# Kernel tuning notes

Hardware: AMD Instinct MI355X
Metric: run time of the kernel (lower is better)

## Reference

```python
import math
import jax, jax.numpy as jnp
import numpy as np

H = 8
DIM = 256
HD = DIM // H
SCALE = math.sqrt(HD)
EPS = 1e-16


def _segment_softmax(scores, dst, num_nodes):
    # scores: [E, H], dst: [E] -> softmax over edges sharing the same dst
    m = jax.ops.segment_max(scores, dst, num_segments=num_nodes)  # [N, H]
    m = jnp.where(jnp.isfinite(m), m, 0.0)  # empty segments -> -inf -> 0
    e = jnp.exp(scores - m[dst])
    s = jax.ops.segment_sum(e, dst, num_segments=num_nodes)  # [N, H]
    return e / (s[dst] + EPS)


def _graph_attention(x, edges, wq, bq, wk, bk, wv, bv, wo, bo):
    # x: [N, DIM]; edges: [2, E] (src, dst). Dropout is identity (eval mode).
    N = x.shape[0]
    Q = (x @ wq + bq).reshape(N, H, HD)
    K = (x @ wk + bk).reshape(N, H, HD)
    V = (x @ wv + bv).reshape(N, H, HD)
    src, dst = edges[0], edges[1]
    scores = jnp.einsum('ehd,ehd->eh', Q[dst], K[src]) / SCALE  # [E, H]
    attn = _segment_softmax(scores, dst, N)  # [E, H]
    msgs = V[src] * attn[:, :, None]  # [E, H, HD]
    out = jax.ops.segment_sum(msgs, dst, num_segments=N).reshape(N, DIM)
    return out @ wo + bo


def _linear_params(key, fan_in, fan_out):
    k1, k2 = jax.random.split(key)
    bound = 1.0 / math.sqrt(fan_in)
    w = jax.random.uniform(k1, (fan_in, fan_out), minval=-bound, maxval=bound, dtype=jnp.float32)
    b = jax.random.uniform(k2, (fan_out,), minval=-bound, maxval=bound, dtype=jnp.float32)
    return w, b


def setup_inputs() -> dict:
    key = jax.random.key(0)
    ks = jax.random.split(key, 12)
    n_slot, n_dom = 20000, 1000
    e_slot, e_dom = 320000, 16000
    inp = {
        'slot_x': jax.random.normal(ks[0], (n_slot, DIM), dtype=jnp.float32),
        'domain_x': jax.random.normal(ks[1], (n_dom, DIM), dtype=jnp.float32),
        'slot_edges': jax.random.randint(ks[2], (2, e_slot), 0, n_slot, dtype=jnp.int32),
        'domain_edges': jax.random.randint(ks[3], (2, e_dom), 0, n_dom, dtype=jnp.int32),
    }
    names = ['wq', 'wk', 'wv', 'wo']
    for i, nm in enumerate(names):
        w, b = _linear_params(ks[4 + i], DIM, DIM)
        inp[f'slot_{nm}'] = w
        inp[f'slot_{nm}_b'] = b
    for i, nm in enumerate(names):
        w, b = _linear_params(ks[8 + i], DIM, DIM)
        inp[f'dom_{nm}'] = w
        inp[f'dom_{nm}_b'] = b
    return inp


def reference(slot_x, domain_x, slot_edges, domain_edges,
              slot_wq, slot_wq_b, slot_wk, slot_wk_b, slot_wv, slot_wv_b, slot_wo, slot_wo_b,
              dom_wq, dom_wq_b, dom_wk, dom_wk_b, dom_wv, dom_wv_b, dom_wo, dom_wo_b):
    # slot branch: self-attention on slot graph + identity residual
    slot_out = _graph_attention(slot_x, slot_edges,
                                slot_wq, slot_wq_b, slot_wk, slot_wk_b,
                                slot_wv, slot_wv_b, slot_wo, slot_wo_b) + slot_x
    # domain branch
    dom_out = _graph_attention(domain_x, domain_edges,
                               dom_wq, dom_wq_b, dom_wk, dom_wk_b,
                               dom_wv, dom_wv_b, dom_wo, dom_wo_b) + domain_x
    return slot_out, dom_out
```

## Files before the change

### kernel.cpp

```cpp
#include <hip/hip_runtime.h>
#include <hip/hip_bf16.h>

#define DIM 256
#define INV_SCALE 0.17677669529663687f
#define SM_EPS 1e-16f
#define BM 128
#define BN 64
#define BK 32

typedef unsigned short ushortT;
typedef unsigned int uintT;
typedef __attribute__((ext_vector_type(8))) __bf16 bf16x8;
typedef __attribute__((ext_vector_type(4))) float f32x4;

__device__ __forceinline__ float bf2f(ushortT u) {
    return __uint_as_float(((uintT)u) << 16);
}
__device__ __forceinline__ ushortT f2bf(float f) {
    uintT u = __float_as_uint(f);
    u += 0x7FFFu + ((u >> 16) & 1u);
    return (ushortT)(u >> 16);
}

struct WPack { const void* w[8]; const void* b[8]; };

__device__ __forceinline__ bool sniff_m16(const ushortT* __restrict__ x) {
    int lane = threadIdx.x & 63;
    ushortT u = x[lane * 2];
    int e = (u >> 7) & 0xFF;
    bool sane = ((u & 0x7FFFu) == 0) || (e >= 0x66 && e <= 0x90);
    unsigned long long m = __ballot(sane);
    return __popcll(m) >= 32;
}

__global__ __launch_bounds__(256) void megaA(
        const void* __restrict__ xs, const void* __restrict__ xd,
        const ushortT* __restrict__ sniff_src,
        ushortT* __restrict__ xb_s, ushortT* __restrict__ xb_d,
        WPack pk, ushortT* __restrict__ wT, float* __restrict__ biasF,
        int* __restrict__ cnt_s, int* __restrict__ cnt_d,
        uintT* __restrict__ st_s, uintT* __restrict__ st_d,
        int* __restrict__ done, int* __restrict__ flagWs,
        int n4s, int n4d, int Ns_, int Nd_, int nbN_, int nbD_,
        int nA0, int nA1, int nA2)
{
    const bool m16 = sniff_m16(sniff_src);
    const int bid = blockIdx.x;
    const int t = threadIdx.x;

    if (bid < nA0 + nA1) {
        const bool d = bid >= nA0;
        const int li = d ? bid - nA0 : bid;
        const int n4 = d ? n4d : n4s;
        const int i = li * 256 + t;
        if (i >= n4) return;
        const void* x = d ? xd : xs;
        ushortT* xb = d ? xb_d : xb_s;
        if (m16) {
            ((ushort4*)xb)[i] = ((const ushort4*)x)[i];
        } else {
            float4 v = ((const float4*)x)[i];
            ushort4 o2;
            o2.x = f2bf(v.x); o2.y = f2bf(v.y); o2.z = f2bf(v.z); o2.w = f2bf(v.w);
            ((ushort4*)xb)[i] = o2;
        }
    } else if (bid < nA0 + nA1 + nA2) {
        const int r = bid - (nA0 + nA1);
        const int which = r / 257;
        const int j = r % 257;
        if (j == 256) {
            const void* b = pk.b[which];
            float v = m16 ? bf2f(((const ushortT*)b)[t]) : ((const float*)b)[t];
            biasF[which * 256 + t] = v;
        } else {
            const void* w = pk.w[which];
            float v = m16 ? bf2f(((const ushortT*)w)[t * 256 + j])
                          : ((const float*)w)[t * 256 + j];
            wT[(size_t)which * 65536 + j * 256 + t] = f2bf(v);
        }
    } else {
        const int li = bid - (nA0 + nA1 + nA2);
        const int idx = li * 256 + t;
        if (idx < Ns_) { cnt_s[idx] = 0; return; }
        int k = idx - Ns_;
        if (k < Nd_) { cnt_d[k] = 0; return; }
        k -= Nd_;
        if (k < nbN_) { st_s[k] = 0; return; }
        k -= nbN_;
        if (k < nbD_) { st_d[k] = 0; return; }
        k -= nbD_;
        if (k == 0) *done = 0;
        else if (k == 1) *flagWs = m16 ? 1 : 0;
    }
}

__device__ __forceinline__ void gemm_core(const ushortT* __restrict__ A,
                                          const ushortT* __restrict__ BT,
                                          int row0, int col0, int M,
                                          f32x4 (&acc)[2][4]) {
    __shared__ ushortT As[BM * BK];
    __shared__ ushortT Bs[BN * BK];
    const int tid  = threadIdx.x;
    const int wid  = tid >> 6;
    const int lane = tid & 63;
    const int r_i = tid >> 2;
    const int kq8 = (tid & 3) << 3;
    const int m   = lane & 15;
    const int q   = lane >> 4;

    const size_t rA0 = (size_t)min(row0 + r_i, M - 1) * DIM;
    const size_t rA1 = (size_t)min(row0 + 64 + r_i, M - 1) * DIM;
    const size_t rB  = (size_t)(col0 + r_i) * DIM;

    for (int k0 = 0; k0 < DIM; k0 += BK) {
        uint4 a0v = *(const uint4*)(A + rA0 + k0 + kq8);
        uint4 a1v = *(const uint4*)(A + rA1 + k0 + kq8);
        uint4 bv  = *(const uint4*)(BT + rB + k0 + kq8);
        __syncthreads();
        *(uint4*)&As[r_i * BK + kq8]        = a0v;
        *(uint4*)&As[(64 + r_i) * BK + kq8] = a1v;
        *(uint4*)&Bs[r_i * BK + kq8]        = bv;
        __syncthreads();

        bf16x8 af0 = *(const bf16x8*)&As[(wid * 32 + m) * BK + q * 8];
        bf16x8 af1 = *(const bf16x8*)&As[(wid * 32 + 16 + m) * BK + q * 8];
        #pragma unroll
        for (int j = 0; j < 4; ++j) {
            bf16x8 bf = *(const bf16x8*)&Bs[(j * 16 + m) * BK + q * 8];
            acc[0][j] = __builtin_amdgcn_mfma_f32_16x16x32_bf16(af0, bf, acc[0][j], 0, 0, 0);
            acc[1][j] = __builtin_amdgcn_mfma_f32_16x16x32_bf16(af1, bf, acc[1][j], 0, 0, 0);
        }
    }
}

__global__ __launch_bounds__(256) void megaB(
        const ushortT* __restrict__ xb_s, const ushortT* __restrict__ xb_d,
        const ushortT* __restrict__ wT, const float* __restrict__ biasF,
        ushortT* __restrict__ qkv_s, ushortT* __restrict__ qkv_d,
        size_t zss, size_t zsd, int Ms, int Md, int nbs_, int nbq_,
        const int* __restrict__ dst_s, const int* __restrict__ dst_d,
        int* __restrict__ cnt_s, int* __restrict__ cnt_d, int Es_, int Ed_)
{
    const int bid = blockIdx.x;
    const int nq = nbq_ * 12;
    if (bid >= nq) {
        const int idx = (bid - nq) * 256 + threadIdx.x;
        if (idx < Es_) atomicAdd(&cnt_s[dst_s[idx]], 1);
        else { int e = idx - Es_; if (e < Ed_) atomicAdd(&cnt_d[dst_d[e]], 1); }
        return;
    }
    const int z  = bid / (nbq_ * 4);
    const int r  = bid % (nbq_ * 4);
    const int by = r / nbq_;
    const int bx0 = r % nbq_;
    const bool dom = bx0 >= nbs_;
    const int bx = dom ? bx0 - nbs_ : bx0;
    const ushortT* A = dom ? xb_d : xb_s;
    const int M = dom ? Md : Ms;
    const int widx = z + (dom ? 4 : 0);
    const ushortT* BT = wT + (size_t)widx * 65536;
    const float* bias = biasF + widx * 256;
    ushortT* C = (dom ? qkv_d : qkv_s) + (size_t)z * (dom ? zsd : zss);

    const int row0 = bx * BM;
    const int col0 = by * BN;
    const int wid = threadIdx.x >> 6, lane = threadIdx.x & 63;
    const int m = lane & 15, q = lane >> 4;

    f32x4 acc[2][4];
    #pragma unroll
    for (int i = 0; i < 2; ++i)
        #pragma unroll
        for (int j = 0; j < 4; ++j) acc[i][j] = (f32x4){0.f, 0.f, 0.f, 0.f};

    gemm_core(A, BT, row0, col0, M, acc);

    #pragma unroll
    for (int i = 0; i < 2; ++i)
        #pragma unroll
        for (int j = 0; j < 4; ++j) {
            const int col = col0 + j * 16 + m;
            const float bval = bias[col];
            #pragma unroll
            for (int rr = 0; rr < 4; ++rr) {
                const int row = row0 + wid * 32 + i * 16 + q * 4 + rr;
                if (row < M)
                    C[(size_t)row * DIM + col] = f2bf(acc[i][j][rr] + bval);
            }
        }
}

__device__ __forceinline__ uintT spack(uintT st, uintT v) { return (st << 30) | v; }

__global__ __launch_bounds__(256) void scan_nodes(
        const int* __restrict__ cnt_s, const int* __restrict__ cnt_d,
        uintT* __restrict__ st_s, uintT* __restrict__ st_d,
        int* __restrict__ rp_s, int* __restrict__ rp_d,
        int* __restrict__ cur_s, int* __restrict__ cur_d,
        int Ns_, int Nd_, int nbN_)
{
    __shared__ int sh[256];
    __shared__ int exclS;
    const int b = blockIdx.x;
    const int t = threadIdx.x;
    const bool dom = b >= nbN_;
    const int lb = dom ? b - nbN_ : b;
    const int N = dom ? Nd_ : Ns_;
    const int* cnt = dom ? cnt_d : cnt_s;
    uintT* st = dom ? st_d : st_s;
    int* rp = dom ? rp_d : rp_s;
    int* cur = dom ? cur_d : cur_s;

    const int i = lb * 256 + t;
    const int v = (i < N) ? cnt[i] : 0;
    sh[t] = v;
    __syncthreads();
    for (int off = 1; off < 256; off <<= 1) {
        int u = (t >= off) ? sh[t - off] : 0;
        __syncthreads();
        sh[t] += u;
        __syncthreads();
    }

    if (t == 0) {
        const uintT agg = (uintT)sh[255];
        uintT excl = 0;
        if (lb == 0) {
            __hip_atomic_store(&st[0], spack(2u, agg), __ATOMIC_RELEASE,
                               __HIP_MEMORY_SCOPE_AGENT);
        } else {
            __hip_atomic_store(&st[lb], spack(1u, agg), __ATOMIC_RELEASE,
                               __HIP_MEMORY_SCOPE_AGENT);
            int j = lb - 1;
            while (j >= 0) {
                uintT s = __hip_atomic_load(&st[j], __ATOMIC_ACQUIRE,
                                            __HIP_MEMORY_SCOPE_AGENT);
                uintT tag = s >> 30;
                if (tag == 2u) { excl += s & 0x3FFFFFFFu; break; }
                if (tag == 1u) { excl += s & 0x3FFFFFFFu; --j; }
            }
            __hip_atomic_store(&st[lb], spack(2u, excl + agg), __ATOMIC_RELEASE,
                               __HIP_MEMORY_SCOPE_AGENT);
        }
        exclS = (int)excl;
    }
    __syncthreads();
    const int excl = exclS;
    if (i < N) {
        const int e = excl + ((t == 0) ? 0 : sh[t - 1]);
        rp[i] = e;
        cur[i] = e;
        if (i == N - 1) rp[N] = e + v;
    }
}

__global__ __launch_bounds__(256) void scatter_edges(
        const int* __restrict__ ss, const int* __restrict__ ds,
        const int* __restrict__ sd, const int* __restrict__ dd,
        int* __restrict__ cur_s, int* __restrict__ cur_d,
        int* __restrict__ col_s, int* __restrict__ col_d,
        int Es_, int Ed_)
{
    const int idx = blockIdx.x * 256 + threadIdx.x;
    if (idx < Es_) {
        int pos = atomicAdd(&cur_s[ds[idx]], 1);
        col_s[pos] = ss[idx];
    } else {
        int e = idx - Es_;
        if (e < Ed_) {
            int pos = atomicAdd(&cur_d[dd[e]], 1);
            col_d[pos] = sd[e];
        }
    }
}

__global__ __launch_bounds__(256) void attn_kernel(
        const ushortT* __restrict__ Qs, const ushortT* __restrict__ Ks,
        const ushortT* __restrict__ Vs, const int* __restrict__ rps,
        const int* __restrict__ css, ushortT* __restrict__ aggs,
        const ushortT* __restrict__ Qd_, const ushortT* __restrict__ Kd_,
        const ushortT* __restrict__ Vd_, const int* __restrict__ rpd,
        const int* __restrict__ csd, ushortT* __restrict__ aggd,
        int Ns_, int Ntot)
{
    const int sub = threadIdx.x & 31;
    const int g = blockIdx.x * 8 + (threadIdx.x >> 5);
    if (g >= Ntot) return;
    const bool dom = g >= Ns_;
    const int d = dom ? g - Ns_ : g;
    const ushortT* Qb = dom ? Qd_ : Qs;
    const ushortT* Kb = dom ? Kd_ : Ks;
    const ushortT* Vb = dom ? Vd_ : Vs;
    const int* rowptr = dom ? rpd : rps;
    const int* colsrc = dom ? csd : css;
    ushortT* aggb = dom ? aggd : aggs;

    const int c8 = sub * 8;
    const size_t cbase = (size_t)d * DIM + c8;

    uint4 qv = *(const uint4*)(Qb + cbase);
    float qf[8];
    qf[0] = bf2f((ushortT)(qv.x & 0xFFFF)); qf[1] = bf2f((ushortT)(qv.x >> 16));
    qf[2] = bf2f((ushortT)(qv.y & 0xFFFF)); qf[3] = bf2f((ushortT)(qv.y >> 16));
    qf[4] = bf2f((ushortT)(qv.z & 0xFFFF)); qf[5] = bf2f((ushortT)(qv.z >> 16));
    qf[6] = bf2f((ushortT)(qv.w & 0xFFFF)); qf[7] = bf2f((ushortT)(qv.w >> 16));

    float acc[8] = {};
    float den = 0.f;

    auto PROC = [&](uint4 kv, uint4 vv) {
        float kf[8];
        kf[0] = bf2f((ushortT)(kv.x & 0xFFFF)); kf[1] = bf2f((ushortT)(kv.x >> 16));
        kf[2] = bf2f((ushortT)(kv.y & 0xFFFF)); kf[3] = bf2f((ushortT)(kv.y >> 16));
        kf[4] = bf2f((ushortT)(kv.z & 0xFFFF)); kf[5] = bf2f((ushortT)(kv.z >> 16));
        kf[6] = bf2f((ushortT)(kv.w & 0xFFFF)); kf[7] = bf2f((ushortT)(kv.w >> 16));
        float p = qf[0] * kf[0] + qf[1] * kf[1] + qf[2] * kf[2] + qf[3] * kf[3]
                + qf[4] * kf[4] + qf[5] * kf[5] + qf[6] * kf[6] + qf[7] * kf[7];
        p += __shfl_xor(p, 1, 4);
        p += __shfl_xor(p, 2, 4);
        const float w = __expf(fminf(p * INV_SCALE, 60.0f));
        den += w;
        acc[0] += w * bf2f((ushortT)(vv.x & 0xFFFF));
        acc[1] += w * bf2f((ushortT)(vv.x >> 16));
        acc[2] += w * bf2f((ushortT)(vv.y & 0xFFFF));
        acc[3] += w * bf2f((ushortT)(vv.y >> 16));
        acc[4] += w * bf2f((ushortT)(vv.z & 0xFFFF));
        acc[5] += w * bf2f((ushortT)(vv.z >> 16));
        acc[6] += w * bf2f((ushortT)(vv.w & 0xFFFF));
        acc[7] += w * bf2f((ushortT)(vv.w >> 16));
    };

    const int beg = rowptr[d], end = rowptr[d + 1];
    int i = beg;
    for (; i + 8 <= end; i += 8) {
        uint4 kv[8], vv[8];
        #pragma unroll
        for (int j = 0; j < 8; ++j) {
            const size_t b = (size_t)colsrc[i + j] * DIM + c8;
            kv[j] = *(const uint4*)(Kb + b);
            vv[j] = *(const uint4*)(Vb + b);
        }
        #pragma unroll
        for (int j = 0; j < 8; ++j) PROC(kv[j], vv[j]);
    }
    for (; i + 4 <= end; i += 4) {
        uint4 kv[4], vv[4];
        #pragma unroll
        for (int j = 0; j < 4; ++j) {
            const size_t b = (size_t)colsrc[i + j] * DIM + c8;
            kv[j] = *(const uint4*)(Kb + b);
            vv[j] = *(const uint4*)(Vb + b);
        }
        #pragma unroll
        for (int j = 0; j < 4; ++j) PROC(kv[j], vv[j]);
    }
    for (; i < end; ++i) {
        const size_t sb = (size_t)colsrc[i] * DIM + c8;
        PROC(*(const uint4*)(Kb + sb), *(const uint4*)(Vb + sb));
    }

    const float r = 1.0f / (den + SM_EPS);
    uint4 o;
    o.x = (uintT)f2bf(acc[0] * r) | ((uintT)f2bf(acc[1] * r) << 16);
    o.y = (uintT)f2bf(acc[2] * r) | ((uintT)f2bf(acc[3] * r) << 16);
    o.z = (uintT)f2bf(acc[4] * r) | ((uintT)f2bf(acc[5] * r) << 16);
    o.w = (uintT)f2bf(acc[6] * r) | ((uintT)f2bf(acc[7] * r) << 16);
    *(uint4*)(aggb + cbase) = o;
}

__global__ __launch_bounds__(256) void gemm_out(
        const ushortT* __restrict__ As_, const ushortT* __restrict__ Ad_,
        const ushortT* __restrict__ wT, const float* __restrict__ biasF,
        const void* __restrict__ xs, const void* __restrict__ xd,
        void* __restrict__ dout, int Ms, int Md, int nbs,
        const int* __restrict__ flag)
{
    const bool dom = (int)blockIdx.x >= nbs;
    const int bx = dom ? blockIdx.x - nbs : blockIdx.x;
    const ushortT* A = dom ? Ad_ : As_;
    const int M = dom ? Md : Ms;
    const int widx = 3 + (dom ? 4 : 0);
    const ushortT* BT = wT + (size_t)widx * 65536;
    const float* bias = biasF + widx * 256;
    const void* res = dom ? xd : xs;
    const size_t outOff = dom ? (size_t)Ms * DIM : 0;

    const int row0 = bx * BM;
    const int col0 = blockIdx.y * BN;
    const int wid = threadIdx.x >> 6, lane = threadIdx.x & 63;
    const int m = lane & 15, q = lane >> 4;

    f32x4 acc[2][4];
    #pragma unroll
    for (int i = 0; i < 2; ++i)
        #pragma unroll
        for (int j = 0; j < 4; ++j) acc[i][j] = (f32x4){0.f, 0.f, 0.f, 0.f};

    gemm_core(A, BT, row0, col0, M, acc);

    const bool m16 = (*flag != 0);
    #pragma unroll
    for (int i = 0; i < 2; ++i)
        #pragma unroll
        for (int j = 0; j < 4; ++j) {
            const int col = col0 + j * 16 + m;
            const float bval = bias[col];
            #pragma unroll
            for (int r = 0; r < 4; ++r) {
                const int row = row0 + wid * 32 + i * 16 + q * 4 + r;
                if (row < M) {
                    const size_t ridx = (size_t)row * DIM + col;
                    float v = acc[i][j][r] + bval;
                    v += m16 ? bf2f(((const ushortT*)res)[ridx])
                             : ((const float*)res)[ridx];
                    if (m16) ((ushortT*)dout)[outOff + ridx] = f2bf(v);
                    else     ((float*)dout)[outOff + ridx] = v;
                }
            }
        }
}

extern "C" void kernel_launch(void* const* d_in, const int* in_sizes, int n_in,
                              void* d_out, int out_size, void* d_ws, size_t ws_size,
                              hipStream_t stream)
{
    const void* slot_x = d_in[0];
    const void* dom_x  = d_in[1];
    const int* slot_edges = (const int*)d_in[2];
    const int* dom_edges  = (const int*)d_in[3];
    const int Ns = in_sizes[0] / DIM;
    const int Nd = in_sizes[1] / DIM;
    const int Es = in_sizes[2] / 2;
    const int Ed = in_sizes[3] / 2;

    WPack pk;
    for (int i = 0; i < 8; ++i) { pk.w[i] = d_in[4 + 2 * i]; pk.b[i] = d_in[5 + 2 * i]; }

    char* p = (char*)d_ws;
    size_t o = 0;
    auto take = [&](size_t b) { void* r = p + o; o = (o + b + 255) & ~(size_t)255; return r; };
    const size_t ndS = (size_t)Ns * DIM;
    const size_t ndD = (size_t)Nd * DIM;
    ushortT* xb_s  = (ushortT*)take(ndS * 2);
    ushortT* qkv_s = (ushortT*)take(3 * ndS * 2);
    ushortT* agg_s = (ushortT*)take(ndS * 2);
    ushortT* xb_d  = (ushortT*)take(ndD * 2);
    ushortT* qkv_d = (ushortT*)take(3 * ndD * 2);
    ushortT* agg_d = (ushortT*)take(ndD * 2);
    ushortT* wT    = (ushortT*)take(8 * 65536 * 2);
    float*   biasF = (float*)take(8 * 256 * 4);
    int* rp_s  = (int*)take((size_t)(Ns + 1) * 4);
    int* cur_s = (int*)take((size_t)Ns * 4);
    int* cnt_s = (int*)take((size_t)Ns * 4);
    int* col_s = (int*)take((size_t)Es * 4);
    int* rp_d  = (int*)take((size_t)(Nd + 1) * 4);
    int* cur_d = (int*)take((size_t)Nd * 4);
    int* cnt_d = (int*)take((size_t)Nd * 4);
    int* col_d = (int*)take((size_t)Ed * 4);
    uintT* st_s = (uintT*)take(512 * 4);
    uintT* st_d = (uintT*)take(256 * 4);
    int* done   = (int*)take(256);
    int* flagWs = (int*)take(256);

    const int* src_s = slot_edges;
    const int* dst_s = slot_edges + Es;
    const int* src_d = dom_edges;
    const int* dst_d = dom_edges + Ed;

    const int n4s = Ns * DIM / 4, n4d = Nd * DIM / 4;
    const int nbN = (Ns + 255) / 256;
    const int nbD = (Nd + 255) / 256;
    const int nbs = (Ns + BM - 1) / BM;
    const int nbd = (Nd + BM - 1) / BM;
    const int nbq = nbs + nbd;

    const int nA0 = (n4s + 255) / 256;
    const int nA1 = (n4d + 255) / 256;
    const int nA2 = 257 * 8;
    const int nZ  = (Ns + Nd + nbN + nbD + 2 + 255) / 256;
    hipLaunchKernelGGL(megaA, dim3(nA0 + nA1 + nA2 + nZ), dim3(256), 0, stream,
                       slot_x, dom_x, (const ushortT*)slot_x, xb_s, xb_d,
                       pk, wT, biasF, cnt_s, cnt_d, st_s, st_d, done, flagWs,
                       n4s, n4d, Ns, Nd, nbN, nbD, nA0, nA1, nA2);

    const int nCnt = (Es + Ed + 255) / 256;
    hipLaunchKernelGGL(megaB, dim3(nbq * 12 + nCnt), dim3(256), 0, stream,
                       xb_s, xb_d, wT, biasF, qkv_s, qkv_d, ndS, ndD,
                       Ns, Nd, nbs, nbq, dst_s, dst_d, cnt_s, cnt_d, Es, Ed);

    hipLaunchKernelGGL(scan_nodes, dim3(nbN + nbD), dim3(256), 0, stream,
                       cnt_s, cnt_d, st_s, st_d, rp_s, rp_d, cur_s, cur_d,
                       Ns, Nd, nbN);
    hipLaunchKernelGGL(scatter_edges, dim3(nCnt), dim3(256), 0, stream,
                       src_s, dst_s, src_d, dst_d, cur_s, cur_d, col_s, col_d,
                       Es, Ed);

    const int Ntot = Ns + Nd;
    hipLaunchKernelGGL(attn_kernel, dim3((Ntot + 7) / 8), dim3(256), 0, stream,
                       qkv_s, qkv_s + ndS, qkv_s + 2 * ndS, rp_s, col_s, agg_s,
                       qkv_d, qkv_d + ndD, qkv_d + 2 * ndD, rp_d, col_d, agg_d,
                       Ns, Ntot);

    hipLaunchKernelGGL(gemm_out, dim3(nbq, DIM / BN), dim3(256), 0, stream,
                       agg_s, agg_d, wT, biasF, slot_x, dom_x, d_out,
                       Ns, Nd, nbs, flagWs);
}
```

Baseline: 274.5 us.

## Fuse QKV GEMMs per block, tile weight transpose, widen attention to wavefront per node

```diff
diff --git a/kernel.cpp b/kernel.cpp
--- a/kernel.cpp
+++ b/kernel.cpp
@@ -42,7 +42,7 @@
         uintT* __restrict__ st_s, uintT* __restrict__ st_d,
         int* __restrict__ done, int* __restrict__ flagWs,
         int n4s, int n4d, int Ns_, int Nd_, int nbN_, int nbD_,
-        int nA0, int nA1, int nA2)
+        int nA0, int nA1)
 {
     const bool m16 = sniff_m16(sniff_src);
     const int bid = blockIdx.x;
@@ -64,22 +64,34 @@
             o2.x = f2bf(v.x); o2.y = f2bf(v.y); o2.z = f2bf(v.z); o2.w = f2bf(v.w);
             ((ushort4*)xb)[i] = o2;
         }
-    } else if (bid < nA0 + nA1 + nA2) {
-        const int r = bid - (nA0 + nA1);
-        const int which = r / 257;
-        const int j = r % 257;
-        if (j == 256) {
-            const void* b = pk.b[which];
-            float v = m16 ? bf2f(((const ushortT*)b)[t]) : ((const float*)b)[t];
-            biasF[which * 256 + t] = v;
-        } else {
-            const void* w = pk.w[which];
-            float v = m16 ? bf2f(((const ushortT*)w)[t * 256 + j])
-                          : ((const float*)w)[t * 256 + j];
-            wT[(size_t)which * 65536 + j * 256 + t] = f2bf(v);
-        }
+    } else if (bid < nA0 + nA1 + 128) {
+        __shared__ float sh[64][65];
+        const int r0 = bid - (nA0 + nA1);
+        const int which = r0 >> 4;
+        const int tile = r0 & 15;
+        const int tr = tile >> 2, tc = tile & 3;
+        const void* w = pk.w[which];
+        const int tx = t & 63, tg = t >> 6;
+        #pragma unroll
+        for (int i = 0; i < 16; ++i) {
+            const int r = i * 4 + tg;
+            const size_t si = (size_t)(tr * 64 + r) * 256 + tc * 64 + tx;
+            sh[r][tx] = m16 ? bf2f(((const ushortT*)w)[si]) : ((const float*)w)[si];
+        }
+        __syncthreads();
+        ushortT* o = wT + (size_t)which * 65536;
+        #pragma unroll
+        for (int i = 0; i < 16; ++i) {
+            const int r = i * 4 + tg;
+            o[(size_t)(tc * 64 + r) * 256 + tr * 64 + tx] = f2bf(sh[tx][r]);
+        }
+    } else if (bid < nA0 + nA1 + 136) {
+        const int which = bid - (nA0 + nA1 + 128);
+        const void* b = pk.b[which];
+        float v = m16 ? bf2f(((const ushortT*)b)[t]) : ((const float*)b)[t];
+        biasF[which * 256 + t] = v;
     } else {
-        const int li = bid - (nA0 + nA1 + nA2);
+        const int li = bid - (nA0 + nA1 + 136);
         const int idx = li * 256 + t;
         if (idx < Ns_) { cnt_s[idx] = 0; return; }
         int k = idx - Ns_;
@@ -94,12 +106,34 @@
     }
 }
 
-__device__ __forceinline__ void gemm_core(const ushortT* __restrict__ A,
-                                          const ushortT* __restrict__ BT,
-                                          int row0, int col0, int M,
-                                          f32x4 (&acc)[2][4]) {
+__global__ __launch_bounds__(256) void megaB(
+        const ushortT* __restrict__ xb_s, const ushortT* __restrict__ xb_d,
+        const ushortT* __restrict__ wT, const float* __restrict__ biasF,
+        ushortT* __restrict__ qkv_s, ushortT* __restrict__ qkv_d,
+        size_t zss, size_t zsd, int Ms, int Md, int nbs_, int nbq_,
+        const int* __restrict__ dst_s, const int* __restrict__ dst_d,
+        int* __restrict__ cnt_s, int* __restrict__ cnt_d, int Es_, int Ed_)
+{
+    const int bid = blockIdx.x;
+    const int nq = nbq_ * 4;
+    if (bid >= nq) {
+        const int idx = (bid - nq) * 256 + threadIdx.x;
+        if (idx < Es_) atomicAdd(&cnt_s[dst_s[idx]], 1);
+        else { int e = idx - Es_; if (e < Ed_) atomicAdd(&cnt_d[dst_d[e]], 1); }
+        return;
+    }
+    const int by  = bid / nbq_;
+    const int bx0 = bid % nbq_;
+    const bool dom = bx0 >= nbs_;
+    const int bx = dom ? bx0 - nbs_ : bx0;
+    const ushortT* A = dom ? xb_d : xb_s;
+    const int M = dom ? Md : Ms;
+    const int wbase = dom ? 4 : 0;
+    const size_t zstride = dom ? zsd : zss;
+    ushortT* Cb = dom ? qkv_d : qkv_s;
+
     __shared__ ushortT As[BM * BK];
-    __shared__ ushortT Bs[BN * BK];
+    __shared__ ushortT Bs[3][BN * BK];
     const int tid  = threadIdx.x;
     const int wid  = tid >> 6;
     const int lane = tid & 63;
@@ -107,6 +141,17 @@
     const int kq8 = (tid & 3) << 3;
     const int m   = lane & 15;
     const int q   = lane >> 4;
+    const int row0 = bx * BM;
+    const int col0 = by * BN;
+
+    f32x4 acc[3][2][4];
+    #pragma unroll
+    for (int z = 0; z < 3; ++z)
+        #pragma unroll
+        for (int i = 0; i < 2; ++i)
+            #pragma unroll
+            for (int j = 0; j < 4; ++j)
+                acc[z][i][j] = (f32x4){0.f, 0.f, 0.f, 0.f};
 
     const size_t rA0 = (size_t)min(row0 + r_i, M - 1) * DIM;
     const size_t rA1 = (size_t)min(row0 + 64 + r_i, M - 1) * DIM;
@@ -115,79 +160,48 @@
     for (int k0 = 0; k0 < DIM; k0 += BK) {
         uint4 a0v = *(const uint4*)(A + rA0 + k0 + kq8);
         uint4 a1v = *(const uint4*)(A + rA1 + k0 + kq8);
-        uint4 bv  = *(const uint4*)(BT + rB + k0 + kq8);
+        uint4 b0v = *(const uint4*)(wT + (size_t)(wbase + 0) * 65536 + rB + k0 + kq8);
+        uint4 b1v = *(const uint4*)(wT + (size_t)(wbase + 1) * 65536 + rB + k0 + kq8);
+        uint4 b2v = *(const uint4*)(wT + (size_t)(wbase + 2) * 65536 + rB + k0 + kq8);
         __syncthreads();
         *(uint4*)&As[r_i * BK + kq8]        = a0v;
         *(uint4*)&As[(64 + r_i) * BK + kq8] = a1v;
-        *(uint4*)&Bs[r_i * BK + kq8]        = bv;
+        *(uint4*)&Bs[0][r_i * BK + kq8]     = b0v;
+        *(uint4*)&Bs[1][r_i * BK + kq8]     = b1v;
+        *(uint4*)&Bs[2][r_i * BK + kq8]     = b2v;
         __syncthreads();
 
         bf16x8 af0 = *(const bf16x8*)&As[(wid * 32 + m) * BK + q * 8];
         bf16x8 af1 = *(const bf16x8*)&As[(wid * 32 + 16 + m) * BK + q * 8];
         #pragma unroll
         for (int j = 0; j < 4; ++j) {
-            bf16x8 bf = *(const bf16x8*)&Bs[(j * 16 + m) * BK + q * 8];
-            acc[0][j] = __builtin_amdgcn_mfma_f32_16x16x32_bf16(af0, bf, acc[0][j], 0, 0, 0);
-            acc[1][j] = __builtin_amdgcn_mfma_f32_16x16x32_bf16(af1, bf, acc[1][j], 0, 0, 0);
-        }
-    }
-}
-
-__global__ __launch_bounds__(256) void megaB(
-        const ushortT* __restrict__ xb_s, const ushortT* __restrict__ xb_d,
-        const ushortT* __restrict__ wT, const float* __restrict__ biasF,
-        ushortT* __restrict__ qkv_s, ushortT* __restrict__ qkv_d,
-        size_t zss, size_t zsd, int Ms, int Md, int nbs_, int nbq_,
-        const int* __restrict__ dst_s, const int* __restrict__ dst_d,
-        int* __restrict__ cnt_s, int* __restrict__ cnt_d, int Es_, int Ed_)
-{
-    const int bid = blockIdx.x;
-    const int nq = nbq_ * 12;
-    if (bid >= nq) {
-        const int idx = (bid - nq) * 256 + threadIdx.x;
-        if (idx < Es_) atomicAdd(&cnt_s[dst_s[idx]], 1);
-        else { int e = idx - Es_; if (e < Ed_) atomicAdd(&cnt_d[dst_d[e]], 1); }
-        return;
-    }
-    const int z  = bid / (nbq_ * 4);
-    const int r  = bid % (nbq_ * 4);
-    const int by = r / nbq_;
-    const int bx0 = r % nbq_;
-    const bool dom = bx0 >= nbs_;
-    const int bx = dom ? bx0 - nbs_ : bx0;
-    const ushortT* A = dom ? xb_d : xb_s;
-    const int M = dom ? Md : Ms;
-    const int widx = z + (dom ? 4 : 0);
-    const ushortT* BT = wT + (size_t)widx * 65536;
-    const float* bias = biasF + widx * 256;
-    ushortT* C = (dom ? qkv_d : qkv_s) + (size_t)z * (dom ? zsd : zss);
-
-    const int row0 = bx * BM;
-    const int col0 = by * BN;
-    const int wid = threadIdx.x >> 6, lane = threadIdx.x & 63;
-    const int m = lane & 15, q = lane >> 4;
-
-    f32x4 acc[2][4];
+            #pragma unroll
+            for (int z = 0; z < 3; ++z) {
+                bf16x8 bf = *(const bf16x8*)&Bs[z][(j * 16 + m) * BK + q * 8];
+                acc[z][0][j] = __builtin_amdgcn_mfma_f32_16x16x32_bf16(af0, bf, acc[z][0][j], 0, 0, 0);
+                acc[z][1][j] = __builtin_amdgcn_mfma_f32_16x16x32_bf16(af1, bf, acc[z][1][j], 0, 0, 0);
+            }
+        }
+    }
+
     #pragma unroll
-    for (int i = 0; i < 2; ++i)
-        #pragma unroll
-        for (int j = 0; j < 4; ++j) acc[i][j] = (f32x4){0.f, 0.f, 0.f, 0.f};
-
-    gemm_core(A, BT, row0, col0, M, acc);
-
-    #pragma unroll
-    for (int i = 0; i < 2; ++i)
-        #pragma unroll
-        for (int j = 0; j < 4; ++j) {
-            const int col = col0 + j * 16 + m;
-            const float bval = bias[col];
+    for (int z = 0; z < 3; ++z) {
+        ushortT* C = Cb + (size_t)z * zstride;
+        const float* bias = biasF + (wbase + z) * 256;
+        #pragma unroll
+        for (int i = 0; i < 2; ++i)
             #pragma unroll
-            for (int rr = 0; rr < 4; ++rr) {
-                const int row = row0 + wid * 32 + i * 16 + q * 4 + rr;
-                if (row < M)
-                    C[(size_t)row * DIM + col] = f2bf(acc[i][j][rr] + bval);
+            for (int j = 0; j < 4; ++j) {
+                const int col = col0 + j * 16 + m;
+                const float bval = bias[col];
+                #pragma unroll
+                for (int rr = 0; rr < 4; ++rr) {
+                    const int row = row0 + wid * 32 + i * 16 + q * 4 + rr;
+                    if (row < M)
+                        C[(size_t)row * DIM + col] = f2bf(acc[z][i][j][rr] + bval);
+                }
             }
-        }
+    }
 }
 
 __device__ __forceinline__ uintT spack(uintT st, uintT v) { return (st << 30) | v; }
@@ -283,11 +297,11 @@
         const int* __restrict__ csd, ushortT* __restrict__ aggd,
         int Ns_, int Ntot)
 {
-    const int sub = threadIdx.x & 31;
-    const int g = blockIdx.x * 8 + (threadIdx.x >> 5);
+    const int g = blockIdx.x * 4 + (threadIdx.x >> 6);
     if (g >= Ntot) return;
     const bool dom = g >= Ns_;
     const int d = dom ? g - Ns_ : g;
+    const int t = threadIdx.x & 63;
     const ushortT* Qb = dom ? Qd_ : Qs;
     const ushortT* Kb = dom ? Kd_ : Ks;
     const ushortT* Vb = dom ? Vd_ : Vs;
@@ -295,77 +309,53 @@
     const int* colsrc = dom ? csd : css;
     ushortT* aggb = dom ? aggd : aggs;
 
-    const int c8 = sub * 8;
-    const size_t cbase = (size_t)d * DIM + c8;
-
-    uint4 qv = *(const uint4*)(Qb + cbase);
-    float qf[8];
-    qf[0] = bf2f((ushortT)(qv.x & 0xFFFF)); qf[1] = bf2f((ushortT)(qv.x >> 16));
-    qf[2] = bf2f((ushortT)(qv.y & 0xFFFF)); qf[3] = bf2f((ushortT)(qv.y >> 16));
-    qf[4] = bf2f((ushortT)(qv.z & 0xFFFF)); qf[5] = bf2f((ushortT)(qv.z >> 16));
-    qf[6] = bf2f((ushortT)(qv.w & 0xFFFF)); qf[7] = bf2f((ushortT)(qv.w >> 16));
-
-    float acc[8] = {};
-    float den = 0.f;
-
-    auto PROC = [&](uint4 kv, uint4 vv) {
-        float kf[8];
-        kf[0] = bf2f((ushortT)(kv.x & 0xFFFF)); kf[1] = bf2f((ushortT)(kv.x >> 16));
-        kf[2] = bf2f((ushortT)(kv.y & 0xFFFF)); kf[3] = bf2f((ushortT)(kv.y >> 16));
-        kf[4] = bf2f((ushortT)(kv.z & 0xFFFF)); kf[5] = bf2f((ushortT)(kv.z >> 16));
-        kf[6] = bf2f((ushortT)(kv.w & 0xFFFF)); kf[7] = bf2f((ushortT)(kv.w >> 16));
-        float p = qf[0] * kf[0] + qf[1] * kf[1] + qf[2] * kf[2] + qf[3] * kf[3]
-                + qf[4] * kf[4] + qf[5] * kf[5] + qf[6] * kf[6] + qf[7] * kf[7];
-        p += __shfl_xor(p, 1, 4);
-        p += __shfl_xor(p, 2, 4);
+    const int t4 = t * 4;
+    const size_t cbase = (size_t)d * DIM + t4;
+    uint2 qv = *(const uint2*)(Qb + cbase);
+    const float q0 = bf2f((ushortT)(qv.x & 0xFFFF)), q1 = bf2f((ushortT)(qv.x >> 16));
+    const float q2 = bf2f((ushortT)(qv.y & 0xFFFF)), q3 = bf2f((ushortT)(qv.y >> 16));
+
+    float a0 = 0.f, a1 = 0.f, a2 = 0.f, a3 = 0.f, den = 0.f;
+
+    auto PROC = [&](uint2 kvc, uint2 vvc) {
+        float k0 = bf2f((ushortT)(kvc.x & 0xFFFF)), k1 = bf2f((ushortT)(kvc.x >> 16));
+        float k2 = bf2f((ushortT)(kvc.y & 0xFFFF)), k3 = bf2f((ushortT)(kvc.y >> 16));
+        float p = q0 * k0 + q1 * k1 + q2 * k2 + q3 * k3;
+        p += __shfl_xor(p, 1, 8);
+        p += __shfl_xor(p, 2, 8);
+        p += __shfl_xor(p, 4, 8);
         const float w = __expf(fminf(p * INV_SCALE, 60.0f));
         den += w;
-        acc[0] += w * bf2f((ushortT)(vv.x & 0xFFFF));
-        acc[1] += w * bf2f((ushortT)(vv.x >> 16));
-        acc[2] += w * bf2f((ushortT)(vv.y & 0xFFFF));
-        acc[3] += w * bf2f((ushortT)(vv.y >> 16));
-        acc[4] += w * bf2f((ushortT)(vv.z & 0xFFFF));
-        acc[5] += w * bf2f((ushortT)(vv.z >> 16));
-        acc[6] += w * bf2f((ushortT)(vv.w & 0xFFFF));
-        acc[7] += w * bf2f((ushortT)(vv.w >> 16));
+        a0 += w * bf2f((ushortT)(vvc.x & 0xFFFF));
+        a1 += w * bf2f((ushortT)(vvc.x >> 16));
+        a2 += w * bf2f((ushortT)(vvc.y & 0xFFFF));
+        a3 += w * bf2f((ushortT)(vvc.y >> 16));
     };
 
     const int beg = rowptr[d], end = rowptr[d + 1];
     int i = beg;
-    for (; i + 8 <= end; i += 8) {
-        uint4 kv[8], vv[8];
-        #pragma unroll
-        for (int j = 0; j < 8; ++j) {
-            const size_t b = (size_t)colsrc[i + j] * DIM + c8;
-            kv[j] = *(const uint4*)(Kb + b);
-            vv[j] = *(const uint4*)(Vb + b);
-        }
-        #pragma unroll
-        for (int j = 0; j < 8; ++j) PROC(kv[j], vv[j]);
-    }
     for (; i + 4 <= end; i += 4) {
-        uint4 kv[4], vv[4];
-        #pragma unroll
-        for (int j = 0; j < 4; ++j) {
-            const size_t b = (size_t)colsrc[i + j] * DIM + c8;
-            kv[j] = *(const uint4*)(Kb + b);
-            vv[j] = *(const uint4*)(Vb + b);
-        }
-        #pragma unroll
-        for (int j = 0; j < 4; ++j) PROC(kv[j], vv[j]);
+        const int s0 = colsrc[i], s1 = colsrc[i + 1];
+        const int s2 = colsrc[i + 2], s3 = colsrc[i + 3];
+        const size_t b0 = (size_t)s0 * DIM + t4, b1 = (size_t)s1 * DIM + t4;
+        const size_t b2 = (size_t)s2 * DIM + t4, b3 = (size_t)s3 * DIM + t4;
+        uint2 k0v = *(const uint2*)(Kb + b0), v0v = *(const uint2*)(Vb + b0);
+        uint2 k1v = *(const uint2*)(Kb + b1), v1v = *(const uint2*)(Vb + b1);
+        uint2 k2v = *(const uint2*)(Kb + b2), v2v = *(const uint2*)(Vb + b2);
+        uint2 k3v = *(const uint2*)(Kb + b3), v3v = *(const uint2*)(Vb + b3);
+        PROC(k0v, v0v); PROC(k1v, v1v); PROC(k2v, v2v); PROC(k3v, v3v);
     }
     for (; i < end; ++i) {
-        const size_t sb = (size_t)colsrc[i] * DIM + c8;
-        PROC(*(const uint4*)(Kb + sb), *(const uint4*)(Vb + sb));
+        const size_t sb = (size_t)colsrc[i] * DIM + t4;
+        uint2 kv = *(const uint2*)(Kb + sb);
+        uint2 vv = *(const uint2*)(Vb + sb);
+        PROC(kv, vv);
     }
 
     const float r = 1.0f / (den + SM_EPS);
-    uint4 o;
-    o.x = (uintT)f2bf(acc[0] * r) | ((uintT)f2bf(acc[1] * r) << 16);
-    o.y = (uintT)f2bf(acc[2] * r) | ((uintT)f2bf(acc[3] * r) << 16);
-    o.z = (uintT)f2bf(acc[4] * r) | ((uintT)f2bf(acc[5] * r) << 16);
-    o.w = (uintT)f2bf(acc[6] * r) | ((uintT)f2bf(acc[7] * r) << 16);
-    *(uint4*)(aggb + cbase) = o;
+    ushort4 o;
+    o.x = f2bf(a0 * r); o.y = f2bf(a1 * r); o.z = f2bf(a2 * r); o.w = f2bf(a3 * r);
+    *(ushort4*)(aggb + cbase) = o;
 }
 
 __global__ __launch_bounds__(256) void gemm_out(
@@ -385,10 +375,17 @@
     const void* res = dom ? xd : xs;
     const size_t outOff = dom ? (size_t)Ms * DIM : 0;
 
+    __shared__ ushortT As2[BM * BK];
+    __shared__ ushortT Bs2[BN * BK];
+    const int tid  = threadIdx.x;
+    const int wid  = tid >> 6;
+    const int lane = tid & 63;
+    const int r_i = tid >> 2;
+    const int kq8 = (tid & 3) << 3;
+    const int m   = lane & 15;
+    const int q   = lane >> 4;
     const int row0 = bx * BM;
     const int col0 = blockIdx.y * BN;
-    const int wid = threadIdx.x >> 6, lane = threadIdx.x & 63;
-    const int m = lane & 15, q = lane >> 4;
 
     f32x4 acc[2][4];
     #pragma unroll
@@ -396,7 +393,29 @@
         #pragma unroll
         for (int j = 0; j < 4; ++j) acc[i][j] = (f32x4){0.f, 0.f, 0.f, 0.f};
 
-    gemm_core(A, BT, row0, col0, M, acc);
+    const size_t rA0 = (size_t)min(row0 + r_i, M - 1) * DIM;
+    const size_t rA1 = (size_t)min(row0 + 64 + r_i, M - 1) * DIM;
+    const size_t rB  = (size_t)(col0 + r_i) * DIM;
+
+    for (int k0 = 0; k0 < DIM; k0 += BK) {
+        uint4 a0v = *(const uint4*)(A + rA0 + k0 + kq8);
+        uint4 a1v = *(const uint4*)(A + rA1 + k0 + kq8);
+        uint4 bv  = *(const uint4*)(BT + rB + k0 + kq8);
+        __syncthreads();
+        *(uint4*)&As2[r_i * BK + kq8]        = a0v;
+        *(uint4*)&As2[(64 + r_i) * BK + kq8] = a1v;
+        *(uint4*)&Bs2[r_i * BK + kq8]        = bv;
+        __syncthreads();
+
+        bf16x8 af0 = *(const bf16x8*)&As2[(wid * 32 + m) * BK + q * 8];
+        bf16x8 af1 = *(const bf16x8*)&As2[(wid * 32 + 16 + m) * BK + q * 8];
+        #pragma unroll
+        for (int j = 0; j < 4; ++j) {
+            bf16x8 bf = *(const bf16x8*)&Bs2[(j * 16 + m) * BK + q * 8];
+            acc[0][j] = __builtin_amdgcn_mfma_f32_16x16x32_bf16(af0, bf, acc[0][j], 0, 0, 0);
+            acc[1][j] = __builtin_amdgcn_mfma_f32_16x16x32_bf16(af1, bf, acc[1][j], 0, 0, 0);
+        }
+    }
 
     const bool m16 = (*flag != 0);
     #pragma unroll
@@ -476,15 +495,14 @@
 
     const int nA0 = (n4s + 255) / 256;
     const int nA1 = (n4d + 255) / 256;
-    const int nA2 = 257 * 8;
     const int nZ  = (Ns + Nd + nbN + nbD + 2 + 255) / 256;
-    hipLaunchKernelGGL(megaA, dim3(nA0 + nA1 + nA2 + nZ), dim3(256), 0, stream,
+    hipLaunchKernelGGL(megaA, dim3(nA0 + nA1 + 136 + nZ), dim3(256), 0, stream,
                        slot_x, dom_x, (const ushortT*)slot_x, xb_s, xb_d,
                        pk, wT, biasF, cnt_s, cnt_d, st_s, st_d, done, flagWs,
-                       n4s, n4d, Ns, Nd, nbN, nbD, nA0, nA1, nA2);
+                       n4s, n4d, Ns, Nd, nbN, nbD, nA0, nA1);
 
     const int nCnt = (Es + Ed + 255) / 256;
-    hipLaunchKernelGGL(megaB, dim3(nbq * 12 + nCnt), dim3(256), 0, stream,
+    hipLaunchKernelGGL(megaB, dim3(nbq * 4 + nCnt), dim3(256), 0, stream,
                        xb_s, xb_d, wT, biasF, qkv_s, qkv_d, ndS, ndD,
                        Ns, Nd, nbs, nbq, dst_s, dst_d, cnt_s, cnt_d, Es, Ed);
 
@@ -496,7 +514,7 @@
                        Es, Ed);
 
     const int Ntot = Ns + Nd;
-    hipLaunchKernelGGL(attn_kernel, dim3((Ntot + 7) / 8), dim3(256), 0, stream,
+    hipLaunchKernelGGL(attn_kernel, dim3((Ntot + 3) / 4), dim3(256), 0, stream,
                        qkv_s, qkv_s + ndS, qkv_s + 2 * ndS, rp_s, col_s, agg_s,
                        qkv_d, qkv_d + ndD, qkv_d + 2 * ndD, rp_d, col_d, agg_d,
                        Ns, Ntot);
```

New measurement: 264.1 us. -3.8%, faster.
